# Kernel optimization log

Measured on AMD Instinct MI355X. Metric: run time of the kernel, lower is better.

Reference implementation:

```python
import jax, jax.numpy as jnp
import numpy as np

B, S, D = 4, 4096, 1024
E, H, TOPK = 8, 2752, 2


def setup_inputs() -> dict:
    key = jax.random.key(0)
    k0, k1, k2, k3, k4 = jax.random.split(key, 5)
    x = jax.random.normal(k0, (B, S, D), dtype=jnp.float32)
    gate_w = jax.random.normal(k1, (E, D), dtype=jnp.float32) * 0.02
    w1 = jax.random.normal(k2, (E, H, D), dtype=jnp.float32) * 0.02
    w2 = jax.random.normal(k3, (E, D, H), dtype=jnp.float32) * 0.02
    w3 = jax.random.normal(k4, (E, H, D), dtype=jnp.float32) * 0.02
    return {"x": x, "gate_w": gate_w, "w1": w1, "w2": w2, "w3": w3}


def reference(x, gate_w, w1, w2, w3):
    """MoE layer: softmax router -> top-k (normalized) -> per-expert SwiGLU FFN -> weighted combine."""
    b, s, d = x.shape
    xt = x.reshape(-1, d)                       # [T, D], T = B*S
    logits = xt @ gate_w.T                      # [T, E]
    scores = jax.nn.softmax(logits, axis=-1)
    topk_w, topk_i = jax.lax.top_k(scores, TOPK)  # [T, K]
    topk_w = topk_w / (jnp.sum(topk_w, axis=-1, keepdims=True) + 1e-20)

    y = jnp.zeros_like(xt)
    n_experts = gate_w.shape[0]
    for e in range(n_experts):
        # combine weight for expert e per token (0 if not routed to e)
        we = jnp.sum(jnp.where(topk_i == e, topk_w, 0.0), axis=-1)  # [T]
        h = jax.nn.silu(xt @ w1[e].T) * (xt @ w3[e].T)              # [T, H]
        y = y + we[:, None] * (h @ w2[e].T)                         # [T, D]
    return y.reshape(b, s, d)
```

## Files before the change

kernel.cpp:

```cpp
#include <hip/hip_runtime.h>
#include <hip/hip_bf16.h>
#include <stdint.h>

#define T_TOK 16384
#define D_DIM 1024
#define E_NUM 8
#define H_DIM 2752
#define NSLOT (T_TOK * 2)

typedef __bf16 bf16x8_t __attribute__((ext_vector_type(8)));
typedef float f32x4_t __attribute__((ext_vector_type(4)));

__device__ __forceinline__ uint16_t f2bf(float f) {
    union { float f; uint32_t u; } v; v.f = f;
    return (uint16_t)((v.u + 0x7FFFu + ((v.u >> 16) & 1u)) >> 16);
}
__device__ __forceinline__ ushort4 f4_to_bf4(float4 v) {
    ushort4 r; r.x = f2bf(v.x); r.y = f2bf(v.y); r.z = f2bf(v.z); r.w = f2bf(v.w);
    return r;
}
__device__ __forceinline__ void gl_lds16(const uint16_t* g, uint16_t* l) {
    __builtin_amdgcn_global_load_lds((const __attribute__((address_space(1))) void*)g,
                                     (__attribute__((address_space(3))) void*)l,
                                     16, 0, 0);
}

__global__ __launch_bounds__(256) void router_kernel(
    const float* __restrict__ x, const float* __restrict__ gw,
    int* __restrict__ topk_i, float* __restrict__ topk_w) {
    int tid = threadIdx.x;
    int t = blockIdx.x * 4 + (tid >> 6);
    int lane = tid & 63;
    const float* xr = x + (size_t)t * D_DIM;
    double acc[E_NUM];
#pragma unroll
    for (int e = 0; e < E_NUM; ++e) acc[e] = 0.0;
    for (int k = lane; k < D_DIM; k += 64) {
        double xv = (double)xr[k];
#pragma unroll
        for (int e = 0; e < E_NUM; ++e) acc[e] += xv * (double)gw[e * D_DIM + k];
    }
#pragma unroll
    for (int e = 0; e < E_NUM; ++e) {
        double v = acc[e];
        for (int off = 32; off > 0; off >>= 1) v += __shfl_down(v, off, 64);
        acc[e] = v;
    }
    if (lane == 0) {
        int i0 = 0; double m0 = acc[0];
#pragma unroll
        for (int e = 1; e < E_NUM; ++e) if (acc[e] > m0) { m0 = acc[e]; i0 = e; }
        int i1 = -1; double m1 = -1.0e300;
#pragma unroll
        for (int e = 0; e < E_NUM; ++e) if (e != i0 && acc[e] > m1) { m1 = acc[e]; i1 = e; }
        double e1 = exp(m1 - m0);
        double s = 1.0 + e1;
        topk_i[t * 2 + 0] = i0; topk_i[t * 2 + 1] = i1;
        topk_w[t * 2 + 0] = (float)(1.0 / s);
        topk_w[t * 2 + 1] = (float)(e1 / s);
    }
}

__global__ __launch_bounds__(256) void count_kernel(
    const int* __restrict__ topk_i,
    int* __restrict__ counts_f, int* __restrict__ counts_s) {
    __shared__ int hf[E_NUM], hs[E_NUM];
    int tid = threadIdx.x;
    if (tid < E_NUM) { hf[tid] = 0; hs[tid] = 0; }
    __syncthreads();
    int t = blockIdx.x * 256 + tid;
    atomicAdd(&hf[topk_i[t * 2 + 0]], 1);
    atomicAdd(&hs[topk_i[t * 2 + 1]], 1);
    __syncthreads();
    if (tid < E_NUM) {
        if (hf[tid]) atomicAdd(&counts_f[tid], hf[tid]);
    } else if (tid < 2 * E_NUM) {
        int e = tid - E_NUM;
        if (hs[e]) atomicAdd(&counts_s[e], hs[e]);
    }
}

__global__ void prefix_kernel(const int* __restrict__ cf, const int* __restrict__ cs,
                              int* __restrict__ bases, int* __restrict__ splits,
                              int* __restrict__ cnts) {
    int s = 0;
    for (int e = 0; e < E_NUM; ++e) {
        bases[e] = s;
        splits[e] = s + cf[e];
        cnts[e] = cf[e] + cs[e];
        s += cnts[e];
    }
}

__global__ __launch_bounds__(256) void assign_kernel(
    const int* __restrict__ topk_i, const float* __restrict__ topk_w,
    const int* __restrict__ bases, const int* __restrict__ splits,
    int* __restrict__ fills_f, int* __restrict__ fills_s,
    int* __restrict__ slot_tok, float* __restrict__ slot_w) {
    __shared__ int hf[E_NUM], hs[E_NUM], bf[E_NUM], bs[E_NUM];
    int tid = threadIdx.x;
    if (tid < E_NUM) { hf[tid] = 0; hs[tid] = 0; }
    __syncthreads();
    int t = blockIdx.x * 256 + tid;
    int e0 = topk_i[t * 2 + 0], e1 = topk_i[t * 2 + 1];
    int r0 = atomicAdd(&hf[e0], 1);
    int r1 = atomicAdd(&hs[e1], 1);
    __syncthreads();
    if (tid < E_NUM) {
        bf[tid] = hf[tid] ? atomicAdd(&fills_f[tid], hf[tid]) : 0;
    } else if (tid < 2 * E_NUM) {
        int e = tid - E_NUM;
        bs[e] = hs[e] ? atomicAdd(&fills_s[e], hs[e]) : 0;
    }
    __syncthreads();
    int s0 = bases[e0] + bf[e0] + r0;
    int s1 = splits[e1] + bs[e1] + r1;
    slot_tok[s0] = t; slot_w[s0] = topk_w[t * 2 + 0];
    slot_tok[s1] = t; slot_w[s1] = topk_w[t * 2 + 1];
}

__global__ __launch_bounds__(256) void cvtx_kernel(const float* __restrict__ x,
                                                   uint16_t* __restrict__ Xb) {
    size_t i = (size_t)blockIdx.x * 256 + threadIdx.x;
    ((ushort4*)Xb)[i] = f4_to_bf4(((const float4*)x)[i]);
}
__global__ __launch_bounds__(256) void cvt13g_kernel(const float* __restrict__ w1,
                                                     const float* __restrict__ w3,
                                                     uint16_t* __restrict__ w1be,
                                                     uint16_t* __restrict__ w3be, int g) {
    size_t i = (size_t)blockIdx.x * 256 + threadIdx.x;
    size_t off = (size_t)g * 4 * H_DIM * D_DIM / 4;
    ((ushort4*)w1be)[i] = f4_to_bf4(((const float4*)w1)[off + i]);
    ((ushort4*)w3be)[i] = f4_to_bf4(((const float4*)w3)[off + i]);
}
__global__ __launch_bounds__(256) void cvt2_kernel(const float* __restrict__ w2,
                                                   uint16_t* __restrict__ w2b) {
    size_t i = (size_t)blockIdx.x * 256 + threadIdx.x;
    ((ushort4*)w2b)[i] = f4_to_bf4(((const float4*)w2)[i]);
}

__global__ __launch_bounds__(256) void gemm1_kernel(
    const uint16_t* __restrict__ Xb, const uint16_t* __restrict__ w1be,
    const uint16_t* __restrict__ w3be, const int* __restrict__ slot_tok,
    const int* __restrict__ cnts, const int* __restrict__ bases,
    uint16_t* __restrict__ hidden, int g) {
    int ez = blockIdx.z;
    int e = g * 4 + ez;
    int cnt = cnts[e];
    int m0 = blockIdx.y * 128;
    if (m0 >= cnt) return;
    int n0 = blockIdx.x * 64;
    int base = bases[e];
    const uint16_t* w1p = w1be + (size_t)ez * H_DIM * D_DIM;
    const uint16_t* w3p = w3be + (size_t)ez * H_DIM * D_DIM;

    __shared__ __align__(16) uint16_t As[128 * 32];
    __shared__ __align__(16) uint16_t B1s[64 * 32];
    __shared__ __align__(16) uint16_t B3s[64 * 32];

    int tid = threadIdx.x;
    int w = tid >> 6, lane = tid & 63;
    int rA = lane & 15, kq = lane >> 4;
    int lr = lane >> 2, lc = lane & 3;

    int tok0 = slot_tok[base + min(m0 + w * 32 + lr, cnt - 1)];
    int tok1 = slot_tok[base + min(m0 + w * 32 + 16 + lr, cnt - 1)];
    const uint16_t* pA0 = Xb + (size_t)tok0 * D_DIM + lc * 8;
    const uint16_t* pA1 = Xb + (size_t)tok1 * D_DIM + lc * 8;
    const uint16_t* pB1 = w1p + (size_t)(n0 + w * 16 + lr) * D_DIM + lc * 8;
    const uint16_t* pB3 = w3p + (size_t)(n0 + w * 16 + lr) * D_DIM + lc * 8;
    uint16_t* lA0 = &As[(w * 2 + 0) * 512];
    uint16_t* lA1 = &As[(w * 2 + 1) * 512];
    uint16_t* lB1 = &B1s[w * 512];
    uint16_t* lB3 = &B3s[w * 512];

    f32x4_t acc1[2][4], acc3[2][4];
#pragma unroll
    for (int r = 0; r < 2; ++r)
#pragma unroll
        for (int n = 0; n < 4; ++n) {
            acc1[r][n] = (f32x4_t){0.f, 0.f, 0.f, 0.f};
            acc3[r][n] = (f32x4_t){0.f, 0.f, 0.f, 0.f};
        }

    for (int k0 = 0; k0 < D_DIM; k0 += 32) {
        __syncthreads();
        gl_lds16(pA0, lA0);
        gl_lds16(pA1, lA1);
        gl_lds16(pB1, lB1);
        gl_lds16(pB3, lB3);
        pA0 += 32; pA1 += 32; pB1 += 32; pB3 += 32;
        __syncthreads();

        bf16x8_t a0 = *(const bf16x8_t*)&As[(w * 32 + rA) * 32 + kq * 8];
        bf16x8_t a1 = *(const bf16x8_t*)&As[(w * 32 + 16 + rA) * 32 + kq * 8];
#pragma unroll
        for (int n = 0; n < 4; ++n) {
            bf16x8_t b1 = *(const bf16x8_t*)&B1s[(n * 16 + rA) * 32 + kq * 8];
            bf16x8_t b3 = *(const bf16x8_t*)&B3s[(n * 16 + rA) * 32 + kq * 8];
            acc1[0][n] = __builtin_amdgcn_mfma_f32_16x16x32_bf16(a0, b1, acc1[0][n], 0, 0, 0);
            acc1[1][n] = __builtin_amdgcn_mfma_f32_16x16x32_bf16(a1, b1, acc1[1][n], 0, 0, 0);
            acc3[0][n] = __builtin_amdgcn_mfma_f32_16x16x32_bf16(a0, b3, acc3[0][n], 0, 0, 0);
            acc3[1][n] = __builtin_amdgcn_mfma_f32_16x16x32_bf16(a1, b3, acc3[1][n], 0, 0, 0);
        }
    }

#pragma unroll
    for (int r = 0; r < 2; ++r)
#pragma unroll
        for (int n = 0; n < 4; ++n)
#pragma unroll
            for (int i = 0; i < 4; ++i) {
                int mrow = m0 + w * 32 + r * 16 + kq * 4 + i;
                if (mrow < cnt) {
                    float gv = acc1[r][n][i];
                    float s = gv / (1.0f + __expf(-gv));
                    float h = s * acc3[r][n][i];
                    hidden[(size_t)(base + mrow) * H_DIM + n0 + n * 16 + rA] = f2bf(h);
                }
            }
}

__global__ __launch_bounds__(256) void gemm2_kernel(
    const uint16_t* __restrict__ hidden, const uint16_t* __restrict__ w2b,
    const int* __restrict__ cnts, const int* __restrict__ bases,
    const int* __restrict__ slot_tok, const float* __restrict__ slot_w,
    float* __restrict__ out) {
    int e = blockIdx.z;
    int cnt = cnts[e];
    int lin = blockIdx.y * 8 + blockIdx.x;
    int c = lin & 7, j = lin >> 3;
    int m_t = (j >> 3) * 8 + c;
    int x_t = j & 7;
    int m0 = m_t * 128;
    if (m0 >= cnt) return;
    int base = bases[e];
    int d0 = x_t * 128;

    __shared__ __align__(16) uint16_t As[128 * 32];
    __shared__ __align__(16) uint16_t Bs[128 * 32];

    int tid = threadIdx.x;
    int w = tid >> 6, lane = tid & 63;
    int rA = lane & 15, kq = lane >> 4;
    int lr = lane >> 2, lc = lane & 3;
    int mh = w & 1, nh = w >> 1;

    int sl0 = base + min(m0 + w * 32 + lr, cnt - 1);
    int sl1 = base + min(m0 + w * 32 + 16 + lr, cnt - 1);
    const uint16_t* pA0 = hidden + (size_t)sl0 * H_DIM + lc * 8;
    const uint16_t* pA1 = hidden + (size_t)sl1 * H_DIM + lc * 8;
    const uint16_t* pB0 = w2b + (size_t)(e * D_DIM + d0 + w * 32 + lr) * H_DIM + lc * 8;
    const uint16_t* pB1 = w2b + (size_t)(e * D_DIM + d0 + w * 32 + 16 + lr) * H_DIM + lc * 8;
    uint16_t* lA0 = &As[(w * 2 + 0) * 512];
    uint16_t* lA1 = &As[(w * 2 + 1) * 512];
    uint16_t* lB0 = &Bs[(w * 2 + 0) * 512];
    uint16_t* lB1 = &Bs[(w * 2 + 1) * 512];

    f32x4_t acc[4][4];
#pragma unroll
    for (int mf = 0; mf < 4; ++mf)
#pragma unroll
        for (int nf = 0; nf < 4; ++nf) acc[mf][nf] = (f32x4_t){0.f, 0.f, 0.f, 0.f};

    for (int k0 = 0; k0 < H_DIM; k0 += 32) {
        __syncthreads();
        gl_lds16(pA0, lA0);
        gl_lds16(pA1, lA1);
        gl_lds16(pB0, lB0);
        gl_lds16(pB1, lB1);
        pA0 += 32; pA1 += 32; pB0 += 32; pB1 += 32;
        __syncthreads();

        bf16x8_t a[4], b[4];
#pragma unroll
        for (int mf = 0; mf < 4; ++mf)
            a[mf] = *(const bf16x8_t*)&As[(mh * 64 + mf * 16 + rA) * 32 + kq * 8];
#pragma unroll
        for (int nf = 0; nf < 4; ++nf)
            b[nf] = *(const bf16x8_t*)&Bs[(nh * 64 + nf * 16 + rA) * 32 + kq * 8];
#pragma unroll
        for (int mf = 0; mf < 4; ++mf)
#pragma unroll
            for (int nf = 0; nf < 4; ++nf)
                acc[mf][nf] = __builtin_amdgcn_mfma_f32_16x16x32_bf16(a[mf], b[nf], acc[mf][nf], 0, 0, 0);
    }

#pragma unroll
    for (int mf = 0; mf < 4; ++mf)
#pragma unroll
        for (int i = 0; i < 4; ++i) {
            int mr = m0 + mh * 64 + mf * 16 + kq * 4 + i;
            if (mr < cnt) {
                int slot = base + mr;
                float wgt = slot_w[slot];
                int tok = slot_tok[slot];
                float* yr = out + (size_t)tok * D_DIM + d0 + nh * 64;
#pragma unroll
                for (int nf = 0; nf < 4; ++nf)
                    atomicAdd(&yr[nf * 16 + rA], wgt * acc[mf][nf][i]);
            }
        }
}

extern "C" void kernel_launch(void* const* d_in, const int* in_sizes, int n_in,
                              void* d_out, int out_size, void* d_ws, size_t ws_size,
                              hipStream_t stream) {
    const float* x  = (const float*)d_in[0];
    const float* gw = (const float*)d_in[1];
    const float* w1 = (const float*)d_in[2];
    const float* w2 = (const float*)d_in[3];
    const float* w3 = (const float*)d_in[4];
    float* out = (float*)d_out;
    char* ws = (char*)d_ws;

    int*   counts_f = (int*)(ws + 0);
    int*   counts_s = (int*)(ws + 256);
    int*   fills_f  = (int*)(ws + 512);
    int*   fills_s  = (int*)(ws + 768);
    int*   bases    = (int*)(ws + 1024);
    int*   splits   = (int*)(ws + 1280);
    int*   cnts     = (int*)(ws + 1536);
    int*   topk_i   = (int*)(ws + 4096);
    float* topk_w   = (float*)(ws + 4096 + 1 * 131072);
    int*   slot_tok = (int*)(ws + 4096 + 2 * 131072);
    float* slot_w   = (float*)(ws + 4096 + 3 * 131072);

    const size_t HID_OFF = 4ull << 20;
    const size_t W_OFF   = HID_OFF + (size_t)NSLOT * H_DIM * 2;
    const size_t W1SZ    = (size_t)H_DIM * D_DIM * 2;
    uint16_t* hidden = (uint16_t*)(ws + HID_OFF);
    uint16_t* w1be   = (uint16_t*)(ws + W_OFF);
    uint16_t* w3be   = (uint16_t*)(ws + W_OFF + 4 * W1SZ);
    uint16_t* w2b    = (uint16_t*)(ws + W_OFF);
    uint16_t* Xb     = (uint16_t*)d_out;

    hipMemsetAsync(ws, 0, 1024, stream);

    router_kernel<<<T_TOK / 4, 256, 0, stream>>>(x, gw, topk_i, topk_w);
    count_kernel<<<T_TOK / 256, 256, 0, stream>>>(topk_i, counts_f, counts_s);
    prefix_kernel<<<1, 1, 0, stream>>>(counts_f, counts_s, bases, splits, cnts);
    assign_kernel<<<T_TOK / 256, 256, 0, stream>>>(topk_i, topk_w, bases, splits,
                                                   fills_f, fills_s, slot_tok, slot_w);
    cvtx_kernel<<<T_TOK * D_DIM / 1024, 256, 0, stream>>>(x, Xb);

    for (int g = 0; g < 2; ++g) {
        cvt13g_kernel<<<H_DIM * 4, 256, 0, stream>>>(w1, w3, w1be, w3be, g);
        gemm1_kernel<<<dim3(H_DIM / 64, 128, 4), 256, 0, stream>>>(
            Xb, w1be, w3be, slot_tok, cnts, bases, hidden, g);
    }

    hipMemsetAsync(out, 0, (size_t)T_TOK * D_DIM * sizeof(float), stream);
    cvt2_kernel<<<E_NUM * D_DIM * H_DIM / 1024, 256, 0, stream>>>(w2, w2b);
    gemm2_kernel<<<dim3(8, 128, E_NUM), 256, 0, stream>>>(
        hidden, w2b, cnts, bases, slot_tok, slot_w, out);
}
```

Measured before the change: 1.240 ms.

## Triple-buffer LDS loads in both expert GEMMs and XOR-swizzle LDS layout

Both grouped GEMM kernels now keep three LDS buffers and issue global-to-LDS loads two k-steps ahead. They use explicit vmcnt waits and a single barrier per iteration in place of two __syncthreads around each load. The global source column is XOR-swizzled by row so the bf16x8 fragment reads from LDS hit fewer bank conflicts. This aims to hide global memory latency behind MFMA work, at the cost of three times the LDS footprint, which may lower occupancy, and hand-written wait counts that must match the number of loads in flight.

After: 1.274 ms. 2.7% more time.

```diff
diff --git a/kernel.cpp b/kernel.cpp
--- a/kernel.cpp
+++ b/kernel.cpp
@@ -138,6 +138,7 @@
     size_t i = (size_t)blockIdx.x * 256 + threadIdx.x;
     ((ushort4*)w2b)[i] = f4_to_bf4(((const float4*)w2)[i]);
 }
+
 
 __global__ __launch_bounds__(256) void gemm1_kernel(
     const uint16_t* __restrict__ Xb, const uint16_t* __restrict__ w1be,
@@ -154,25 +155,23 @@
     const uint16_t* w1p = w1be + (size_t)ez * H_DIM * D_DIM;
     const uint16_t* w3p = w3be + (size_t)ez * H_DIM * D_DIM;
 
-    __shared__ __align__(16) uint16_t As[128 * 32];
-    __shared__ __align__(16) uint16_t B1s[64 * 32];
-    __shared__ __align__(16) uint16_t B3s[64 * 32];
+    __shared__ __align__(16) uint16_t As[3][128 * 32];
+    __shared__ __align__(16) uint16_t B1s[3][64 * 32];
+    __shared__ __align__(16) uint16_t B3s[3][64 * 32];
 
     int tid = threadIdx.x;
     int w = tid >> 6, lane = tid & 63;
     int rA = lane & 15, kq = lane >> 4;
     int lr = lane >> 2, lc = lane & 3;
+    int slr = (lr >> 1) & 3;
+    int ks = kq ^ ((rA >> 1) & 3);
 
     int tok0 = slot_tok[base + min(m0 + w * 32 + lr, cnt - 1)];
     int tok1 = slot_tok[base + min(m0 + w * 32 + 16 + lr, cnt - 1)];
-    const uint16_t* pA0 = Xb + (size_t)tok0 * D_DIM + lc * 8;
-    const uint16_t* pA1 = Xb + (size_t)tok1 * D_DIM + lc * 8;
-    const uint16_t* pB1 = w1p + (size_t)(n0 + w * 16 + lr) * D_DIM + lc * 8;
-    const uint16_t* pB3 = w3p + (size_t)(n0 + w * 16 + lr) * D_DIM + lc * 8;
-    uint16_t* lA0 = &As[(w * 2 + 0) * 512];
-    uint16_t* lA1 = &As[(w * 2 + 1) * 512];
-    uint16_t* lB1 = &B1s[w * 512];
-    uint16_t* lB3 = &B3s[w * 512];
+    const uint16_t* pA0 = Xb + (size_t)tok0 * D_DIM + (lc ^ slr) * 8;
+    const uint16_t* pA1 = Xb + (size_t)tok1 * D_DIM + (lc ^ slr) * 8;
+    const uint16_t* pB1 = w1p + (size_t)(n0 + w * 16 + lr) * D_DIM + (lc ^ slr) * 8;
+    const uint16_t* pB3 = w3p + (size_t)(n0 + w * 16 + lr) * D_DIM + (lc ^ slr) * 8;
 
     f32x4_t acc1[2][4], acc3[2][4];
 #pragma unroll
@@ -183,27 +182,35 @@
             acc3[r][n] = (f32x4_t){0.f, 0.f, 0.f, 0.f};
         }
 
-    for (int k0 = 0; k0 < D_DIM; k0 += 32) {
-        __syncthreads();
-        gl_lds16(pA0, lA0);
-        gl_lds16(pA1, lA1);
-        gl_lds16(pB1, lB1);
-        gl_lds16(pB3, lB3);
-        pA0 += 32; pA1 += 32; pB1 += 32; pB3 += 32;
-        __syncthreads();
-
-        bf16x8_t a0 = *(const bf16x8_t*)&As[(w * 32 + rA) * 32 + kq * 8];
-        bf16x8_t a1 = *(const bf16x8_t*)&As[(w * 32 + 16 + rA) * 32 + kq * 8];
+#define G1_STAGE(bi) do {                                   \
+        gl_lds16(pA0, &As[bi][(w * 2 + 0) * 512]);          \
+        gl_lds16(pA1, &As[bi][(w * 2 + 1) * 512]);          \
+        gl_lds16(pB1, &B1s[bi][w * 512]);                   \
+        gl_lds16(pB3, &B3s[bi][w * 512]);                   \
+        pA0 += 32; pA1 += 32; pB1 += 32; pB3 += 32; } while (0)
+
+    G1_STAGE(0);
+    G1_STAGE(1);
+    for (int t = 0; t < 32; ++t) {
+        if (t < 31) { asm volatile("s_waitcnt vmcnt(4)" ::: "memory"); }
+        else        { asm volatile("s_waitcnt vmcnt(0)" ::: "memory"); }
+        __builtin_amdgcn_s_barrier();
+        if (t < 30) G1_STAGE((t + 2) % 3);
+        int c = t % 3;
+
+        bf16x8_t a0 = *(const bf16x8_t*)&As[c][(w * 32 + rA) * 32 + ks * 8];
+        bf16x8_t a1 = *(const bf16x8_t*)&As[c][(w * 32 + 16 + rA) * 32 + ks * 8];
 #pragma unroll
         for (int n = 0; n < 4; ++n) {
-            bf16x8_t b1 = *(const bf16x8_t*)&B1s[(n * 16 + rA) * 32 + kq * 8];
-            bf16x8_t b3 = *(const bf16x8_t*)&B3s[(n * 16 + rA) * 32 + kq * 8];
+            bf16x8_t b1 = *(const bf16x8_t*)&B1s[c][(n * 16 + rA) * 32 + ks * 8];
+            bf16x8_t b3 = *(const bf16x8_t*)&B3s[c][(n * 16 + rA) * 32 + ks * 8];
             acc1[0][n] = __builtin_amdgcn_mfma_f32_16x16x32_bf16(a0, b1, acc1[0][n], 0, 0, 0);
             acc1[1][n] = __builtin_amdgcn_mfma_f32_16x16x32_bf16(a1, b1, acc1[1][n], 0, 0, 0);
             acc3[0][n] = __builtin_amdgcn_mfma_f32_16x16x32_bf16(a0, b3, acc3[0][n], 0, 0, 0);
             acc3[1][n] = __builtin_amdgcn_mfma_f32_16x16x32_bf16(a1, b3, acc3[1][n], 0, 0, 0);
         }
     }
+#undef G1_STAGE
 
 #pragma unroll
     for (int r = 0; r < 2; ++r)
@@ -229,33 +236,31 @@
     int e = blockIdx.z;
     int cnt = cnts[e];
     int lin = blockIdx.y * 8 + blockIdx.x;
-    int c = lin & 7, j = lin >> 3;
-    int m_t = (j >> 3) * 8 + c;
+    int c8 = lin & 7, j = lin >> 3;
+    int m_t = (j >> 3) * 8 + c8;
     int x_t = j & 7;
     int m0 = m_t * 128;
     if (m0 >= cnt) return;
     int base = bases[e];
     int d0 = x_t * 128;
 
-    __shared__ __align__(16) uint16_t As[128 * 32];
-    __shared__ __align__(16) uint16_t Bs[128 * 32];
+    __shared__ __align__(16) uint16_t As[3][128 * 32];
+    __shared__ __align__(16) uint16_t Bs[3][128 * 32];
 
     int tid = threadIdx.x;
     int w = tid >> 6, lane = tid & 63;
     int rA = lane & 15, kq = lane >> 4;
     int lr = lane >> 2, lc = lane & 3;
+    int slr = (lr >> 1) & 3;
+    int ks = kq ^ ((rA >> 1) & 3);
     int mh = w & 1, nh = w >> 1;
 
     int sl0 = base + min(m0 + w * 32 + lr, cnt - 1);
     int sl1 = base + min(m0 + w * 32 + 16 + lr, cnt - 1);
-    const uint16_t* pA0 = hidden + (size_t)sl0 * H_DIM + lc * 8;
-    const uint16_t* pA1 = hidden + (size_t)sl1 * H_DIM + lc * 8;
-    const uint16_t* pB0 = w2b + (size_t)(e * D_DIM + d0 + w * 32 + lr) * H_DIM + lc * 8;
-    const uint16_t* pB1 = w2b + (size_t)(e * D_DIM + d0 + w * 32 + 16 + lr) * H_DIM + lc * 8;
-    uint16_t* lA0 = &As[(w * 2 + 0) * 512];
-    uint16_t* lA1 = &As[(w * 2 + 1) * 512];
-    uint16_t* lB0 = &Bs[(w * 2 + 0) * 512];
-    uint16_t* lB1 = &Bs[(w * 2 + 1) * 512];
+    const uint16_t* pA0 = hidden + (size_t)sl0 * H_DIM + (lc ^ slr) * 8;
+    const uint16_t* pA1 = hidden + (size_t)sl1 * H_DIM + (lc ^ slr) * 8;
+    const uint16_t* pB0 = w2b + (size_t)(e * D_DIM + d0 + w * 32 + lr) * H_DIM + (lc ^ slr) * 8;
+    const uint16_t* pB1 = w2b + (size_t)(e * D_DIM + d0 + w * 32 + 16 + lr) * H_DIM + (lc ^ slr) * 8;
 
     f32x4_t acc[4][4];
 #pragma unroll
@@ -263,28 +268,36 @@
 #pragma unroll
         for (int nf = 0; nf < 4; ++nf) acc[mf][nf] = (f32x4_t){0.f, 0.f, 0.f, 0.f};
 
-    for (int k0 = 0; k0 < H_DIM; k0 += 32) {
-        __syncthreads();
-        gl_lds16(pA0, lA0);
-        gl_lds16(pA1, lA1);
-        gl_lds16(pB0, lB0);
-        gl_lds16(pB1, lB1);
-        pA0 += 32; pA1 += 32; pB0 += 32; pB1 += 32;
-        __syncthreads();
+#define G2_STAGE(bi) do {                                   \
+        gl_lds16(pA0, &As[bi][(w * 2 + 0) * 512]);          \
+        gl_lds16(pA1, &As[bi][(w * 2 + 1) * 512]);          \
+        gl_lds16(pB0, &Bs[bi][(w * 2 + 0) * 512]);          \
+        gl_lds16(pB1, &Bs[bi][(w * 2 + 1) * 512]);          \
+        pA0 += 32; pA1 += 32; pB0 += 32; pB1 += 32; } while (0)
+
+    G2_STAGE(0);
+    G2_STAGE(1);
+    for (int t = 0; t < 86; ++t) {
+        if (t < 85) { asm volatile("s_waitcnt vmcnt(4)" ::: "memory"); }
+        else        { asm volatile("s_waitcnt vmcnt(0)" ::: "memory"); }
+        __builtin_amdgcn_s_barrier();
+        if (t < 84) G2_STAGE((t + 2) % 3);
+        int c = t % 3;
 
         bf16x8_t a[4], b[4];
 #pragma unroll
         for (int mf = 0; mf < 4; ++mf)
-            a[mf] = *(const bf16x8_t*)&As[(mh * 64 + mf * 16 + rA) * 32 + kq * 8];
+            a[mf] = *(const bf16x8_t*)&As[c][(mh * 64 + mf * 16 + rA) * 32 + ks * 8];
 #pragma unroll
         for (int nf = 0; nf < 4; ++nf)
-            b[nf] = *(const bf16x8_t*)&Bs[(nh * 64 + nf * 16 + rA) * 32 + kq * 8];
+            b[nf] = *(const bf16x8_t*)&Bs[c][(nh * 64 + nf * 16 + rA) * 32 + ks * 8];
 #pragma unroll
         for (int mf = 0; mf < 4; ++mf)
 #pragma unroll
             for (int nf = 0; nf < 4; ++nf)
                 acc[mf][nf] = __builtin_amdgcn_mfma_f32_16x16x32_bf16(a[mf], b[nf], acc[mf][nf], 0, 0, 0);
     }
+#undef G2_STAGE
 
 #pragma unroll
     for (int mf = 0; mf < 4; ++mf)
```

## Process experts in pairs, interleaving weight conversion with both GEMMs

Applied to the files above, without the earlier changes.

Restructures the schedule so each pair of experts gets its w1/w3 converted, runs gemm1, then converts w2 and runs gemm2, instead of converting all w2 at once after every gemm1. The bf16 weight staging buffers shrink to two experts and are reused, and Xb moves from the output buffer into the workspace. The aim is a smaller working set that stays resident in cache between each conversion and its GEMM. The cost is more kernel launches and smaller grids per launch, which can leave the GPU underfilled, since gemm2 now launches only two experts' worth of tiles at a time.

Result: slower. 1.270 ms (+2.4%).

```diff
diff --git a/kernel.cpp b/kernel.cpp
--- a/kernel.cpp
+++ b/kernel.cpp
@@ -124,28 +124,29 @@
     size_t i = (size_t)blockIdx.x * 256 + threadIdx.x;
     ((ushort4*)Xb)[i] = f4_to_bf4(((const float4*)x)[i]);
 }
-__global__ __launch_bounds__(256) void cvt13g_kernel(const float* __restrict__ w1,
+__global__ __launch_bounds__(256) void cvt13p_kernel(const float* __restrict__ w1,
                                                      const float* __restrict__ w3,
                                                      uint16_t* __restrict__ w1be,
-                                                     uint16_t* __restrict__ w3be, int g) {
+                                                     uint16_t* __restrict__ w3be, int p) {
     size_t i = (size_t)blockIdx.x * 256 + threadIdx.x;
-    size_t off = (size_t)g * 4 * H_DIM * D_DIM / 4;
+    size_t off = (size_t)p * 2 * H_DIM * D_DIM / 4;
     ((ushort4*)w1be)[i] = f4_to_bf4(((const float4*)w1)[off + i]);
     ((ushort4*)w3be)[i] = f4_to_bf4(((const float4*)w3)[off + i]);
 }
-__global__ __launch_bounds__(256) void cvt2_kernel(const float* __restrict__ w2,
-                                                   uint16_t* __restrict__ w2b) {
+__global__ __launch_bounds__(256) void cvt2p_kernel(const float* __restrict__ w2,
+                                                    uint16_t* __restrict__ w2b, int p) {
     size_t i = (size_t)blockIdx.x * 256 + threadIdx.x;
-    ((ushort4*)w2b)[i] = f4_to_bf4(((const float4*)w2)[i]);
+    size_t off = (size_t)p * 2 * D_DIM * H_DIM / 4;
+    ((ushort4*)w2b)[i] = f4_to_bf4(((const float4*)w2)[off + i]);
 }
 
 __global__ __launch_bounds__(256) void gemm1_kernel(
     const uint16_t* __restrict__ Xb, const uint16_t* __restrict__ w1be,
     const uint16_t* __restrict__ w3be, const int* __restrict__ slot_tok,
     const int* __restrict__ cnts, const int* __restrict__ bases,
-    uint16_t* __restrict__ hidden, int g) {
+    uint16_t* __restrict__ hidden, int p) {
     int ez = blockIdx.z;
-    int e = g * 4 + ez;
+    int e = p * 2 + ez;
     int cnt = cnts[e];
     int m0 = blockIdx.y * 128;
     if (m0 >= cnt) return;
@@ -225,12 +226,13 @@
     const uint16_t* __restrict__ hidden, const uint16_t* __restrict__ w2b,
     const int* __restrict__ cnts, const int* __restrict__ bases,
     const int* __restrict__ slot_tok, const float* __restrict__ slot_w,
-    float* __restrict__ out) {
-    int e = blockIdx.z;
+    float* __restrict__ out, int p) {
+    int ez = blockIdx.z;
+    int e = p * 2 + ez;
     int cnt = cnts[e];
     int lin = blockIdx.y * 8 + blockIdx.x;
-    int c = lin & 7, j = lin >> 3;
-    int m_t = (j >> 3) * 8 + c;
+    int c8 = lin & 7, j = lin >> 3;
+    int m_t = (j >> 3) * 8 + c8;
     int x_t = j & 7;
     int m0 = m_t * 128;
     if (m0 >= cnt) return;
@@ -250,8 +252,8 @@
     int sl1 = base + min(m0 + w * 32 + 16 + lr, cnt - 1);
     const uint16_t* pA0 = hidden + (size_t)sl0 * H_DIM + lc * 8;
     const uint16_t* pA1 = hidden + (size_t)sl1 * H_DIM + lc * 8;
-    const uint16_t* pB0 = w2b + (size_t)(e * D_DIM + d0 + w * 32 + lr) * H_DIM + lc * 8;
-    const uint16_t* pB1 = w2b + (size_t)(e * D_DIM + d0 + w * 32 + 16 + lr) * H_DIM + lc * 8;
+    const uint16_t* pB0 = w2b + (size_t)(ez * D_DIM + d0 + w * 32 + lr) * H_DIM + lc * 8;
+    const uint16_t* pB1 = w2b + (size_t)(ez * D_DIM + d0 + w * 32 + 16 + lr) * H_DIM + lc * 8;
     uint16_t* lA0 = &As[(w * 2 + 0) * 512];
     uint16_t* lA1 = &As[(w * 2 + 1) * 512];
     uint16_t* lB0 = &Bs[(w * 2 + 0) * 512];
@@ -326,16 +328,17 @@
     int*   slot_tok = (int*)(ws + 4096 + 2 * 131072);
     float* slot_w   = (float*)(ws + 4096 + 3 * 131072);
 
-    const size_t HID_OFF = 4ull << 20;
+    const size_t HID_OFF = 1ull << 20;
     const size_t W_OFF   = HID_OFF + (size_t)NSLOT * H_DIM * 2;
-    const size_t W1SZ    = (size_t)H_DIM * D_DIM * 2;
+    const size_t WPAIR   = (size_t)2 * H_DIM * D_DIM * 2;
     uint16_t* hidden = (uint16_t*)(ws + HID_OFF);
     uint16_t* w1be   = (uint16_t*)(ws + W_OFF);
-    uint16_t* w3be   = (uint16_t*)(ws + W_OFF + 4 * W1SZ);
+    uint16_t* w3be   = (uint16_t*)(ws + W_OFF + WPAIR);
     uint16_t* w2b    = (uint16_t*)(ws + W_OFF);
-    uint16_t* Xb     = (uint16_t*)d_out;
+    uint16_t* Xb     = (uint16_t*)(ws + W_OFF + 2 * WPAIR);
 
     hipMemsetAsync(ws, 0, 1024, stream);
+    hipMemsetAsync(out, 0, (size_t)T_TOK * D_DIM * sizeof(float), stream);
 
     router_kernel<<<T_TOK / 4, 256, 0, stream>>>(x, gw, topk_i, topk_w);
     count_kernel<<<T_TOK / 256, 256, 0, stream>>>(topk_i, counts_f, counts_s);
@@ -344,14 +347,12 @@
                                                    fills_f, fills_s, slot_tok, slot_w);
     cvtx_kernel<<<T_TOK * D_DIM / 1024, 256, 0, stream>>>(x, Xb);
 
-    for (int g = 0; g < 2; ++g) {
-        cvt13g_kernel<<<H_DIM * 4, 256, 0, stream>>>(w1, w3, w1be, w3be, g);
-        gemm1_kernel<<<dim3(H_DIM / 64, 128, 4), 256, 0, stream>>>(
-            Xb, w1be, w3be, slot_tok, cnts, bases, hidden, g);
-    }
-
-    hipMemsetAsync(out, 0, (size_t)T_TOK * D_DIM * sizeof(float), stream);
-    cvt2_kernel<<<E_NUM * D_DIM * H_DIM / 1024, 256, 0, stream>>>(w2, w2b);
-    gemm2_kernel<<<dim3(8, 128, E_NUM), 256, 0, stream>>>(
-        hidden, w2b, cnts, bases, slot_tok, slot_w, out);
-}
+    for (int p = 0; p < 4; ++p) {
+        cvt13p_kernel<<<H_DIM * 2, 256, 0, stream>>>(w1, w3, w1be, w3be, p);
+        gemm1_kernel<<<dim3(H_DIM / 64, 128, 2), 256, 0, stream>>>(
+            Xb, w1be, w3be, slot_tok, cnts, bases, hidden, p);
+        cvt2p_kernel<<<H_DIM * 2, 256, 0, stream>>>(w2, w2b, p);
+        gemm2_kernel<<<dim3(8, 128, 2), 256, 0, stream>>>(
+            hidden, w2b, cnts, bases, slot_tok, slot_w, out, p);
+    }
+}
```

## Double the GEMM K-tile to 64 and XOR-swizzle LDS chunks

Applied to the files above, without the earlier changes.

Both expert GEMM kernels now stage a 64-wide K slice per iteration instead of 32. Each iteration issues more direct global-to-LDS loads and runs two MFMA sub-steps. The 16-byte chunks within each LDS row are XOR-swizzled by row pair, and the reads un-swizzle them. This halves the number of barrier pairs per tile and is meant to avoid LDS bank conflicts on the wider rows. The cost is double the shared-memory footprint per block, which may lower occupancy.

Measured after the change: 1.198 ms. 3.4% less time.

```diff
diff --git a/kernel.cpp b/kernel.cpp
--- a/kernel.cpp
+++ b/kernel.cpp
@@ -138,6 +138,7 @@
     size_t i = (size_t)blockIdx.x * 256 + threadIdx.x;
     ((ushort4*)w2b)[i] = f4_to_bf4(((const float4*)w2)[i]);
 }
+
 
 __global__ __launch_bounds__(256) void gemm1_kernel(
     const uint16_t* __restrict__ Xb, const uint16_t* __restrict__ w1be,
@@ -154,25 +155,34 @@
     const uint16_t* w1p = w1be + (size_t)ez * H_DIM * D_DIM;
     const uint16_t* w3p = w3be + (size_t)ez * H_DIM * D_DIM;
 
-    __shared__ __align__(16) uint16_t As[128 * 32];
-    __shared__ __align__(16) uint16_t B1s[64 * 32];
-    __shared__ __align__(16) uint16_t B3s[64 * 32];
+    __shared__ __align__(16) uint16_t As[128 * 64];
+    __shared__ __align__(16) uint16_t B1s[64 * 64];
+    __shared__ __align__(16) uint16_t B3s[64 * 64];
 
     int tid = threadIdx.x;
     int w = tid >> 6, lane = tid & 63;
     int rA = lane & 15, kq = lane >> 4;
-    int lr = lane >> 2, lc = lane & 3;
-
-    int tok0 = slot_tok[base + min(m0 + w * 32 + lr, cnt - 1)];
-    int tok1 = slot_tok[base + min(m0 + w * 32 + 16 + lr, cnt - 1)];
-    const uint16_t* pA0 = Xb + (size_t)tok0 * D_DIM + lc * 8;
-    const uint16_t* pA1 = Xb + (size_t)tok1 * D_DIM + lc * 8;
-    const uint16_t* pB1 = w1p + (size_t)(n0 + w * 16 + lr) * D_DIM + lc * 8;
-    const uint16_t* pB3 = w3p + (size_t)(n0 + w * 16 + lr) * D_DIM + lc * 8;
-    uint16_t* lA0 = &As[(w * 2 + 0) * 512];
-    uint16_t* lA1 = &As[(w * 2 + 1) * 512];
-    uint16_t* lB1 = &B1s[w * 512];
-    uint16_t* lB3 = &B3s[w * 512];
+    int r8 = lane >> 3;
+    int srcc = (lane & 7) ^ ((w * 4 + (lane >> 4)) & 7);
+    int xr = (rA >> 1) & 7;
+
+    const uint16_t *pA0, *pA1, *pA2, *pA3, *pB1, *pB3;
+    {
+        int sr = w * 8 + r8;
+        int t0 = slot_tok[base + min(m0 + 0 * 32 + sr, cnt - 1)];
+        int t1 = slot_tok[base + min(m0 + 1 * 32 + sr, cnt - 1)];
+        int t2 = slot_tok[base + min(m0 + 2 * 32 + sr, cnt - 1)];
+        int t3 = slot_tok[base + min(m0 + 3 * 32 + sr, cnt - 1)];
+        pA0 = Xb + (size_t)t0 * D_DIM + srcc * 8;
+        pA1 = Xb + (size_t)t1 * D_DIM + srcc * 8;
+        pA2 = Xb + (size_t)t2 * D_DIM + srcc * 8;
+        pA3 = Xb + (size_t)t3 * D_DIM + srcc * 8;
+        pB1 = w1p + (size_t)(n0 + sr) * D_DIM + srcc * 8;
+        pB3 = w3p + (size_t)(n0 + sr) * D_DIM + srcc * 8;
+    }
+    uint16_t* lA = &As[(w * 8) * 64];
+    uint16_t* lB1 = &B1s[(w * 8) * 64];
+    uint16_t* lB3 = &B3s[(w * 8) * 64];
 
     f32x4_t acc1[2][4], acc3[2][4];
 #pragma unroll
@@ -183,25 +193,33 @@
             acc3[r][n] = (f32x4_t){0.f, 0.f, 0.f, 0.f};
         }
 
-    for (int k0 = 0; k0 < D_DIM; k0 += 32) {
+    for (int k0 = 0; k0 < D_DIM; k0 += 64) {
         __syncthreads();
-        gl_lds16(pA0, lA0);
-        gl_lds16(pA1, lA1);
+        gl_lds16(pA0, lA);
+        gl_lds16(pA1, lA + 32 * 64);
+        gl_lds16(pA2, lA + 64 * 64);
+        gl_lds16(pA3, lA + 96 * 64);
         gl_lds16(pB1, lB1);
+        gl_lds16(pB1 + 32 * D_DIM, lB1 + 32 * 64);
         gl_lds16(pB3, lB3);
-        pA0 += 32; pA1 += 32; pB1 += 32; pB3 += 32;
+        gl_lds16(pB3 + 32 * D_DIM, lB3 + 32 * 64);
+        pA0 += 64; pA1 += 64; pA2 += 64; pA3 += 64; pB1 += 64; pB3 += 64;
         __syncthreads();
 
-        bf16x8_t a0 = *(const bf16x8_t*)&As[(w * 32 + rA) * 32 + kq * 8];
-        bf16x8_t a1 = *(const bf16x8_t*)&As[(w * 32 + 16 + rA) * 32 + kq * 8];
-#pragma unroll
-        for (int n = 0; n < 4; ++n) {
-            bf16x8_t b1 = *(const bf16x8_t*)&B1s[(n * 16 + rA) * 32 + kq * 8];
-            bf16x8_t b3 = *(const bf16x8_t*)&B3s[(n * 16 + rA) * 32 + kq * 8];
-            acc1[0][n] = __builtin_amdgcn_mfma_f32_16x16x32_bf16(a0, b1, acc1[0][n], 0, 0, 0);
-            acc1[1][n] = __builtin_amdgcn_mfma_f32_16x16x32_bf16(a1, b1, acc1[1][n], 0, 0, 0);
-            acc3[0][n] = __builtin_amdgcn_mfma_f32_16x16x32_bf16(a0, b3, acc3[0][n], 0, 0, 0);
-            acc3[1][n] = __builtin_amdgcn_mfma_f32_16x16x32_bf16(a1, b3, acc3[1][n], 0, 0, 0);
+#pragma unroll
+        for (int kk = 0; kk < 2; ++kk) {
+            int ck = ((kk * 4 + kq) ^ xr) * 8;
+            bf16x8_t a0 = *(const bf16x8_t*)&As[(w * 32 + rA) * 64 + ck];
+            bf16x8_t a1 = *(const bf16x8_t*)&As[(w * 32 + 16 + rA) * 64 + ck];
+#pragma unroll
+            for (int n = 0; n < 4; ++n) {
+                bf16x8_t b1 = *(const bf16x8_t*)&B1s[(n * 16 + rA) * 64 + ck];
+                bf16x8_t b3 = *(const bf16x8_t*)&B3s[(n * 16 + rA) * 64 + ck];
+                acc1[0][n] = __builtin_amdgcn_mfma_f32_16x16x32_bf16(a0, b1, acc1[0][n], 0, 0, 0);
+                acc1[1][n] = __builtin_amdgcn_mfma_f32_16x16x32_bf16(a1, b1, acc1[1][n], 0, 0, 0);
+                acc3[0][n] = __builtin_amdgcn_mfma_f32_16x16x32_bf16(a0, b3, acc3[0][n], 0, 0, 0);
+                acc3[1][n] = __builtin_amdgcn_mfma_f32_16x16x32_bf16(a1, b3, acc3[1][n], 0, 0, 0);
+            }
         }
     }
 
@@ -229,33 +247,40 @@
     int e = blockIdx.z;
     int cnt = cnts[e];
     int lin = blockIdx.y * 8 + blockIdx.x;
-    int c = lin & 7, j = lin >> 3;
-    int m_t = (j >> 3) * 8 + c;
+    int c8 = lin & 7, j = lin >> 3;
+    int m_t = (j >> 3) * 8 + c8;
     int x_t = j & 7;
     int m0 = m_t * 128;
     if (m0 >= cnt) return;
     int base = bases[e];
     int d0 = x_t * 128;
 
-    __shared__ __align__(16) uint16_t As[128 * 32];
-    __shared__ __align__(16) uint16_t Bs[128 * 32];
+    __shared__ __align__(16) uint16_t As[128 * 64];
+    __shared__ __align__(16) uint16_t Bs[128 * 64];
 
     int tid = threadIdx.x;
     int w = tid >> 6, lane = tid & 63;
     int rA = lane & 15, kq = lane >> 4;
-    int lr = lane >> 2, lc = lane & 3;
+    int r8 = lane >> 3;
+    int srcc = (lane & 7) ^ ((w * 4 + (lane >> 4)) & 7);
+    int xr = (rA >> 1) & 7;
     int mh = w & 1, nh = w >> 1;
 
-    int sl0 = base + min(m0 + w * 32 + lr, cnt - 1);
-    int sl1 = base + min(m0 + w * 32 + 16 + lr, cnt - 1);
-    const uint16_t* pA0 = hidden + (size_t)sl0 * H_DIM + lc * 8;
-    const uint16_t* pA1 = hidden + (size_t)sl1 * H_DIM + lc * 8;
-    const uint16_t* pB0 = w2b + (size_t)(e * D_DIM + d0 + w * 32 + lr) * H_DIM + lc * 8;
-    const uint16_t* pB1 = w2b + (size_t)(e * D_DIM + d0 + w * 32 + 16 + lr) * H_DIM + lc * 8;
-    uint16_t* lA0 = &As[(w * 2 + 0) * 512];
-    uint16_t* lA1 = &As[(w * 2 + 1) * 512];
-    uint16_t* lB0 = &Bs[(w * 2 + 0) * 512];
-    uint16_t* lB1 = &Bs[(w * 2 + 1) * 512];
+    const uint16_t *pA0, *pA1, *pA2, *pA3, *pB;
+    {
+        int sr = w * 8 + r8;
+        int s0 = base + min(m0 + 0 * 32 + sr, cnt - 1);
+        int s1 = base + min(m0 + 1 * 32 + sr, cnt - 1);
+        int s2 = base + min(m0 + 2 * 32 + sr, cnt - 1);
+        int s3 = base + min(m0 + 3 * 32 + sr, cnt - 1);
+        pA0 = hidden + (size_t)s0 * H_DIM + srcc * 8;
+        pA1 = hidden + (size_t)s1 * H_DIM + srcc * 8;
+        pA2 = hidden + (size_t)s2 * H_DIM + srcc * 8;
+        pA3 = hidden + (size_t)s3 * H_DIM + srcc * 8;
+        pB = w2b + (size_t)(e * D_DIM + d0 + sr) * H_DIM + srcc * 8;
+    }
+    uint16_t* lA = &As[(w * 8) * 64];
+    uint16_t* lB = &Bs[(w * 8) * 64];
 
     f32x4_t acc[4][4];
 #pragma unroll
@@ -263,27 +288,35 @@
 #pragma unroll
         for (int nf = 0; nf < 4; ++nf) acc[mf][nf] = (f32x4_t){0.f, 0.f, 0.f, 0.f};
 
-    for (int k0 = 0; k0 < H_DIM; k0 += 32) {
+    for (int k0 = 0; k0 < H_DIM; k0 += 64) {
         __syncthreads();
-        gl_lds16(pA0, lA0);
-        gl_lds16(pA1, lA1);
-        gl_lds16(pB0, lB0);
-        gl_lds16(pB1, lB1);
-        pA0 += 32; pA1 += 32; pB0 += 32; pB1 += 32;
+        gl_lds16(pA0, lA);
+        gl_lds16(pA1, lA + 32 * 64);
+        gl_lds16(pA2, lA + 64 * 64);
+        gl_lds16(pA3, lA + 96 * 64);
+        gl_lds16(pB, lB);
+        gl_lds16(pB + 32 * H_DIM, lB + 32 * 64);
+        gl_lds16(pB + 64 * H_DIM, lB + 64 * 64);
+        gl_lds16(pB + 96 * H_DIM, lB + 96 * 64);
+        pA0 += 64; pA1 += 64; pA2 += 64; pA3 += 64; pB += 64;
         __syncthreads();
 
-        bf16x8_t a[4], b[4];
-#pragma unroll
-        for (int mf = 0; mf < 4; ++mf)
-            a[mf] = *(const bf16x8_t*)&As[(mh * 64 + mf * 16 + rA) * 32 + kq * 8];
-#pragma unroll
-        for (int nf = 0; nf < 4; ++nf)
-            b[nf] = *(const bf16x8_t*)&Bs[(nh * 64 + nf * 16 + rA) * 32 + kq * 8];
-#pragma unroll
-        for (int mf = 0; mf < 4; ++mf)
+#pragma unroll
+        for (int kk = 0; kk < 2; ++kk) {
+            int ck = ((kk * 4 + kq) ^ xr) * 8;
+            bf16x8_t a[4], b[4];
+#pragma unroll
+            for (int mf = 0; mf < 4; ++mf)
+                a[mf] = *(const bf16x8_t*)&As[(mh * 64 + mf * 16 + rA) * 64 + ck];
 #pragma unroll
             for (int nf = 0; nf < 4; ++nf)
-                acc[mf][nf] = __builtin_amdgcn_mfma_f32_16x16x32_bf16(a[mf], b[nf], acc[mf][nf], 0, 0, 0);
+                b[nf] = *(const bf16x8_t*)&Bs[(nh * 64 + nf * 16 + rA) * 64 + ck];
+#pragma unroll
+            for (int mf = 0; mf < 4; ++mf)
+#pragma unroll
+                for (int nf = 0; nf < 4; ++nf)
+                    acc[mf][nf] = __builtin_amdgcn_mfma_f32_16x16x32_bf16(a[mf], b[nf], acc[mf][nf], 0, 0, 0);
+        }
     }
 
 #pragma unroll
```
